# Kernel optimization log

Hardware: AMD Instinct MI355X
Metric: run time of the kernel (lower is better)

The kernel has to match this reference:

```python
import jax, jax.numpy as jnp
import numpy as np

N_NODES = 100000
N_EDGES = 1000000
VOCAB = 128
EMB = 64
HID = 64
N_CLASSES = 2
N_GRAPHS = 2048


def setup_inputs() -> dict:
    key = jax.random.key(0)
    ks = jax.random.split(key, 12)
    x = jax.random.randint(ks[0], (N_NODES,), 0, VOCAB)
    edge_index = jax.random.randint(ks[1], (2, N_EDGES), 0, N_NODES)
    batch = jnp.sort(jax.random.randint(ks[2], (N_NODES,), 0, N_GRAPHS))

    def glorot(k, shape):
        fan = shape[0]
        return jax.random.normal(k, shape, dtype=jnp.float32) / np.sqrt(fan).astype(np.float32)

    emb = jax.random.normal(ks[3], (VOCAB, EMB), dtype=jnp.float32)
    W1_l = glorot(ks[4], (EMB, HID)); b1 = jnp.zeros((HID,), jnp.float32)
    W1_r = glorot(ks[5], (EMB, HID))
    W2_l = glorot(ks[6], (HID, HID)); b2 = jnp.zeros((HID,), jnp.float32)
    W2_r = glorot(ks[7], (HID, HID))
    W_out = glorot(ks[8], (HID, N_CLASSES)); b_out = jnp.zeros((N_CLASSES,), jnp.float32)
    return {"x": x, "edge_index": edge_index, "batch": batch, "emb": emb,
            "W1_l": W1_l, "b1": b1, "W1_r": W1_r,
            "W2_l": W2_l, "b2": b2, "W2_r": W2_r,
            "W_out": W_out, "b_out": b_out}


def _sage_conv(h, src, dst, Wl, bl, Wr):
    # PyG SAGEConv: out = lin_l(mean_{j in N(i)} h_j) + lin_r(h_i); lin_r has no bias
    msgs = h[src]                                                        # [E, D] gather
    agg = jax.ops.segment_sum(msgs, dst, num_segments=N_NODES)          # [N, D] scatter-add
    cnt = jax.ops.segment_sum(jnp.ones((src.shape[0], 1), h.dtype), dst,
                              num_segments=N_NODES)                      # [N, 1] degree
    mean = agg / jnp.maximum(cnt, 1.0)
    return mean @ Wl + bl + h @ Wr


def reference(x, edge_index, batch, emb, W1_l, b1, W1_r, W2_l, b2, W2_r, W_out, b_out):
    src, dst = edge_index[0], edge_index[1]
    h = emb[x]                                                           # [N, EMB]
    h = jax.nn.relu(_sage_conv(h, src, dst, W1_l, b1, W1_r))             # [N, HID]
    h = jax.nn.relu(_sage_conv(h, src, dst, W2_l, b2, W2_r))             # [N, HID]
    # global_mean_pool over graph ids
    gsum = jax.ops.segment_sum(h, batch, num_segments=N_GRAPHS)          # [G, HID]
    gcnt = jax.ops.segment_sum(jnp.ones((N_NODES, 1), h.dtype), batch,
                               num_segments=N_GRAPHS)
    pooled = gsum / jnp.maximum(gcnt, 1.0)
    return pooled @ W_out + b_out                                        # [G, C]
```

## Files before the change

### kernel.cpp

```cpp
#include <hip/hip_runtime.h>
#include <hip/hip_bf16.h>

#define N_NODES 100000
#define N_EDGES 1000000
#define EMB 64
#define HID 64
#define VOCAB 128
#define N_GRAPHS 2048

#define CBUCKET 1024
#define NBK ((N_NODES + CBUCKET - 1) / CBUCKET)
#define CAP 16384
#define CHUNK 4096
#define SCAT_BLOCKS ((N_EDGES + CHUNK - 1) / CHUNK)
#define GB ((N_NODES + 255) / 256)

#define BCASTF(v, l) __int_as_float(__builtin_amdgcn_readlane(__float_as_int(v), (l)))

typedef __attribute__((ext_vector_type(8))) short short8;
typedef __attribute__((ext_vector_type(4))) float f32x4;

__device__ __forceinline__ float bf2f(unsigned short u) {
    return __uint_as_float((unsigned)u << 16);
}
__device__ __forceinline__ unsigned short f2bf(float f) {
    return __bfloat16_as_ushort(__float2bfloat16(f));
}

__global__ __launch_bounds__(256) void setup_kernel(
    const int* __restrict__ batch, int* __restrict__ gstart,
    const float* __restrict__ emb, const float* __restrict__ W1l,
    const float* __restrict__ W1r,
    const float* __restrict__ W2l, const float* __restrict__ W2r,
    float* __restrict__ embW1l, float* __restrict__ embW1r,
    unsigned short* __restrict__ w2frag,
    int* __restrict__ cursor, float* __restrict__ gsum)
{
    int b = blockIdx.x;
    int t = threadIdx.x;
    if (b < GB) {
        int i = b * 256 + t;
        if (i >= N_NODES) return;
        int bg = batch[i];
        int bp = (i == 0) ? -1 : batch[i - 1];
        for (int g = bp + 1; g <= bg; ++g) gstart[g] = i;
        if (i == N_NODES - 1)
            for (int g = bg + 1; g <= N_GRAPHS; ++g) gstart[g] = N_NODES;
    } else if (b < GB + 32) {
        int vb = b - GB;
        int wave = t >> 6, lane = t & 63;
        int v = vb * 4 + wave;
        if (v < VOCAB) {
            float er = emb[v * 64 + lane];
            float al = 0.f, ar = 0.f;
#pragma unroll 8
            for (int d = 0; d < 64; ++d) {
                float e = BCASTF(er, d);
                al += e * W1l[d * 64 + lane];
                ar += e * W1r[d * 64 + lane];
            }
            embW1l[v * 64 + lane] = al;
            embW1r[v * 64 + lane] = ar;
        }
        int g = vb * 256 + t;
        int j = g & 7, l = (g >> 3) & 63, h = (g >> 9) & 1, tt = g >> 10;
        int k = h * 32 + ((l >> 4) * 8) + j;
        int n = tt * 16 + (l & 15);
        float w = (n < 64) ? W2l[k * 64 + n] : W2r[k * 64 + (n - 64)];
        w2frag[g] = f2bf(w);
    } else {
        if (t < NBK) cursor[t] = t * CAP;
        for (int i = t; i < N_GRAPHS * 2; i += 256) gsum[i] = 0.f;
    }
}

__global__ __launch_bounds__(256) void scatter_kernel(
    const int* __restrict__ src, const int* __restrict__ dst,
    int* __restrict__ cursor, unsigned* __restrict__ edge8)
{
    __shared__ unsigned earr[CHUNK];
    __shared__ unsigned char karr[CHUNK];
    __shared__ int bcnt[NBK];
    __shared__ int bbase[NBK];
    int t = threadIdx.x;
    if (t < NBK) bcnt[t] = 0;
    __syncthreads();
    int e0 = blockIdx.x * CHUNK;
    int n = min(e0 + CHUNK, N_EDGES) - e0;
    for (int i = t; i < n; i += 256) {
        int d = dst[e0 + i];
        int s = src[e0 + i];
        int k = d >> 10;
        earr[i] = (unsigned)s | ((unsigned)(d & 1023) << 17);
        karr[i] = (unsigned char)k;
        atomicAdd(&bcnt[k], 1);
    }
    __syncthreads();
    if (t < NBK) {
        int c = bcnt[t];
        bbase[t] = c ? atomicAdd(&cursor[t], c) : 0;
        bcnt[t] = 0;
    }
    __syncthreads();
    for (int i = t; i < n; i += 256) {
        int k = karr[i];
        int off = atomicAdd(&bcnt[k], 1);
        edge8[bbase[k] + off] = earr[i];
    }
}

__global__ __launch_bounds__(256) void csr_kernel(
    const unsigned* __restrict__ edge8, const int* __restrict__ cursor,
    int* __restrict__ row_start, int* __restrict__ deg, int* __restrict__ col)
{
    __shared__ int cnt[CBUCKET];
    __shared__ int ssum[256];
    int b = blockIdx.x;
    int t = threadIdx.x;
    int lo = b * CAP, hi = cursor[b];
    for (int i = t; i < CBUCKET; i += 256) cnt[i] = 0;
    __syncthreads();
    for (int i = lo + t; i < hi; i += 256)
        atomicAdd(&cnt[edge8[i] >> 17], 1);
    __syncthreads();
    int v[4]; int sum = 0;
#pragma unroll
    for (int i = 0; i < 4; ++i) { v[i] = cnt[t * 4 + i]; sum += v[i]; }
    ssum[t] = sum;
    __syncthreads();
    for (int off = 1; off < 256; off <<= 1) {
        int tmp = (t >= off) ? ssum[t - off] : 0;
        __syncthreads();
        ssum[t] += tmp;
        __syncthreads();
    }
    int run = ssum[t] - sum;
    int ex0 = run, ex1 = ex0 + v[0], ex2 = ex1 + v[1], ex3 = ex2 + v[2];
    int node = b * CBUCKET + t * 4;
    if (node + 3 < N_NODES) {
        *(int4*)&row_start[node] = make_int4(lo + ex0, lo + ex1, lo + ex2, lo + ex3);
        *(int4*)&deg[node]       = make_int4(v[0], v[1], v[2], v[3]);
    } else {
        int ex[4] = {ex0, ex1, ex2, ex3};
        for (int i = 0; i < 4; ++i)
            if (node + i < N_NODES) { row_start[node + i] = lo + ex[i]; deg[node + i] = v[i]; }
    }
    cnt[t * 4 + 0] = ex0; cnt[t * 4 + 1] = ex1;
    cnt[t * 4 + 2] = ex2; cnt[t * 4 + 3] = ex3;
    __syncthreads();
    for (int i = lo + t; i < hi; i += 256) {
        unsigned e = edge8[i];
        int slot = atomicAdd(&cnt[e >> 17], 1);
        col[lo + slot] = (int)(e & 0x1FFFF);
    }
}

#define S1_NPW 8
__global__ __launch_bounds__(256) void sage1_kernel(
    const int* __restrict__ x, const float* __restrict__ embW1l,
    const float* __restrict__ embW1r, const float* __restrict__ b1,
    const int* __restrict__ row_start, const int* __restrict__ deg,
    const int* __restrict__ col, unsigned short* __restrict__ h1b)
{
    __shared__ float elds[VOCAB * 64];
    int t = threadIdx.x;
    for (int i = t * 4; i < VOCAB * 64; i += 1024)
        *(float4*)&elds[i] = *(const float4*)&embW1l[i];
    __syncthreads();

    int wave = t >> 6, lane = t & 63;
    int base_node = (blockIdx.x * 4 + wave) * S1_NPW;
    float bias = b1[lane];

    int rs[S1_NPW], dgs[S1_NPW], cidx[S1_NPW], xv[S1_NPW], xn[S1_NPW];
    float self[S1_NPW];
#pragma unroll
    for (int n = 0; n < S1_NPW; ++n) {
        rs[n] = row_start[base_node + n];
        dgs[n] = deg[base_node + n];
        xn[n] = x[base_node + n];
    }
#pragma unroll
    for (int n = 0; n < S1_NPW; ++n)
        cidx[n] = (lane < dgs[n]) ? col[rs[n] + lane] : 0;
#pragma unroll
    for (int n = 0; n < S1_NPW; ++n) {
        xv[n] = (lane < dgs[n]) ? x[cidx[n]] : 0;
        self[n] = embW1r[xn[n] * 64 + lane];
    }

    for (int n = 0; n < S1_NPW; ++n) {
        int node = base_node + n;
        int dg = dgs[n];
        int dgc = (dg < 64) ? dg : 64;

        float s0 = 0.f, s1 = 0.f, s2 = 0.f, s3 = 0.f;
        int j = 0;
        for (; j + 4 <= dgc; j += 4) {
            int x0 = __builtin_amdgcn_readlane(xv[n], j + 0);
            int x1 = __builtin_amdgcn_readlane(xv[n], j + 1);
            int x2 = __builtin_amdgcn_readlane(xv[n], j + 2);
            int x3 = __builtin_amdgcn_readlane(xv[n], j + 3);
            s0 += elds[x0 * 64 + lane];
            s1 += elds[x1 * 64 + lane];
            s2 += elds[x2 * 64 + lane];
            s3 += elds[x3 * 64 + lane];
        }
        for (; j < dgc; ++j) {
            int x0 = __builtin_amdgcn_readlane(xv[n], j);
            s0 += elds[x0 * 64 + lane];
        }
        for (int k = 64; k < dg; ++k) {
            int c = col[rs[n] + k];
            s0 += elds[x[c] * 64 + lane];
        }
        float mean = ((s0 + s1) + (s2 + s3)) / fmaxf((float)dg, 1.0f);
        h1b[node * 64 + lane] = f2bf(fmaxf(mean + bias + self[n], 0.f));
    }
}

__global__ __launch_bounds__(256) void mfma_transform_kernel(
    const unsigned short* __restrict__ h1b,
    const unsigned short* __restrict__ w2frag,
    unsigned char* __restrict__ p8, unsigned short* __restrict__ q16)
{
    int wave = threadIdx.x >> 6, lane = threadIdx.x & 63;
    int base16 = blockIdx.x * 64 + wave * 16;
    if (base16 >= N_NODES) return;
    int m = lane & 15, quad = lane >> 4;

    const unsigned short* arow = h1b + (base16 + m) * 64 + quad * 8;
    short8 a0 = *(const short8*)(arow);
    short8 a1 = *(const short8*)(arow + 32);

#pragma unroll
    for (int tt = 0; tt < 8; ++tt) {
        short8 b0 = *(const short8*)(w2frag + (tt * 1024 + 0)   + lane * 8);
        short8 b1 = *(const short8*)(w2frag + (tt * 1024 + 512) + lane * 8);
        f32x4 acc = {0.f, 0.f, 0.f, 0.f};
        acc = __builtin_amdgcn_mfma_f32_16x16x32_bf16(a0, b0, acc, 0, 0, 0);
        acc = __builtin_amdgcn_mfma_f32_16x16x32_bf16(a1, b1, acc, 0, 0, 0);
        int o = tt * 16 + m;
        if (o < 64) {
            int pk01 = __builtin_amdgcn_cvt_pk_fp8_f32(acc[0], acc[1], 0, false);
            int pk23 = __builtin_amdgcn_cvt_pk_fp8_f32(acc[2], acc[3], 0, false);
            p8[(base16 + quad * 4 + 0) * 64 + o] = (unsigned char)(pk01 & 0xff);
            p8[(base16 + quad * 4 + 1) * 64 + o] = (unsigned char)((pk01 >> 8) & 0xff);
            p8[(base16 + quad * 4 + 2) * 64 + o] = (unsigned char)(pk23 & 0xff);
            p8[(base16 + quad * 4 + 3) * 64 + o] = (unsigned char)((pk23 >> 8) & 0xff);
        } else {
            int oc = o & 63;
#pragma unroll
            for (int i = 0; i < 4; ++i) {
                int node = base16 + quad * 4 + i;
                q16[node * 64 + oc] = f2bf(acc[i]);
            }
        }
    }
}

#define S2_NPW 8
__global__ __launch_bounds__(256, 6) void sage2_kernel(
    const unsigned char* __restrict__ p, const unsigned short* __restrict__ q,
    const int* __restrict__ row_start, const int* __restrict__ deg,
    const int* __restrict__ col, const float* __restrict__ b2,
    const float* __restrict__ Wout, const int* __restrict__ batch,
    float* __restrict__ gsum)
{
    int t = threadIdx.x;
    int wave = t >> 6, lane = t & 63;
    int base_node = (blockIdx.x * 4 + wave) * S2_NPW;
    int c = lane & 15;
    int g = lane >> 4;

    float4 b2v = ((const float4*)b2)[c];
    float4 w01 = ((const float4*)Wout)[c * 2];
    float4 w23 = ((const float4*)Wout)[c * 2 + 1];

    int rs[S2_NPW], dgs[S2_NPW], cidx[S2_NPW];
#pragma unroll
    for (int n = 0; n < S2_NPW; ++n) {
        rs[n] = row_start[base_node + n];
        dgs[n] = deg[base_node + n];
    }
#pragma unroll
    for (int n = 0; n < S2_NPW; ++n)
        cidx[n] = (lane < dgs[n]) ? col[rs[n] + lane] : 0;

    for (int n = 0; n < S2_NPW; ++n) {
        int node = base_node + n;
        int dg = dgs[n];
        int dgc = (dg < 64) ? dg : 64;

        float4 a0 = {0.f,0.f,0.f,0.f}, a1 = {0.f,0.f,0.f,0.f};
        for (int j = 0; j < dgc; j += 8) {
            int jj0 = j + g, jj1 = j + 4 + g;
            int i0 = __shfl(cidx[n], jj0, 64);
            int i1 = __shfl(cidx[n], jj1, 64);
            unsigned v0 = *(const unsigned*)(p + i0 * 64 + c * 4);
            unsigned v1 = *(const unsigned*)(p + i1 * 64 + c * 4);
            if (jj0 < dgc) {
                a0.x += __builtin_amdgcn_cvt_f32_fp8(v0, 0);
                a0.y += __builtin_amdgcn_cvt_f32_fp8(v0, 1);
                a0.z += __builtin_amdgcn_cvt_f32_fp8(v0, 2);
                a0.w += __builtin_amdgcn_cvt_f32_fp8(v0, 3);
            }
            if (jj1 < dgc) {
                a1.x += __builtin_amdgcn_cvt_f32_fp8(v1, 0);
                a1.y += __builtin_amdgcn_cvt_f32_fp8(v1, 1);
                a1.z += __builtin_amdgcn_cvt_f32_fp8(v1, 2);
                a1.w += __builtin_amdgcn_cvt_f32_fp8(v1, 3);
            }
        }
        for (int k = 64; k < dg; ++k) {
            int r = col[rs[n] + k];
            unsigned v = *(const unsigned*)(p + r * 64 + c * 4);
            if (g == 0) {
                a0.x += __builtin_amdgcn_cvt_f32_fp8(v, 0);
                a0.y += __builtin_amdgcn_cvt_f32_fp8(v, 1);
                a0.z += __builtin_amdgcn_cvt_f32_fp8(v, 2);
                a0.w += __builtin_amdgcn_cvt_f32_fp8(v, 3);
            }
        }
        float sx = a0.x + a1.x, sy = a0.y + a1.y, sz = a0.z + a1.z, sw = a0.w + a1.w;
        sx += __shfl_xor(sx, 16, 64); sx += __shfl_xor(sx, 32, 64);
        sy += __shfl_xor(sy, 16, 64); sy += __shfl_xor(sy, 32, 64);
        sz += __shfl_xor(sz, 16, 64); sz += __shfl_xor(sz, 32, 64);
        sw += __shfl_xor(sw, 16, 64); sw += __shfl_xor(sw, 32, 64);

        float inv = 1.0f / fmaxf((float)dg, 1.0f);
        ushort4 qv = *(const ushort4*)(q + node * 64 + c * 4);
        float h0 = fmaxf(sx * inv + b2v.x + bf2f(qv.x), 0.f);
        float h1 = fmaxf(sy * inv + b2v.y + bf2f(qv.y), 0.f);
        float h2 = fmaxf(sz * inv + b2v.z + bf2f(qv.z), 0.f);
        float h3 = fmaxf(sw * inv + b2v.w + bf2f(qv.w), 0.f);

        float p0 = h0 * w01.x + h1 * w01.z + h2 * w23.x + h3 * w23.z;
        float p1 = h0 * w01.y + h1 * w01.w + h2 * w23.y + h3 * w23.w;
        if (g != 0) { p0 = 0.f; p1 = 0.f; }
        p0 += __shfl_down(p0, 8, 64);  p1 += __shfl_down(p1, 8, 64);
        p0 += __shfl_down(p0, 4, 64);  p1 += __shfl_down(p1, 4, 64);
        p0 += __shfl_down(p0, 2, 64);  p1 += __shfl_down(p1, 2, 64);
        p0 += __shfl_down(p0, 1, 64);  p1 += __shfl_down(p1, 1, 64);
        if (lane == 0) {
            int grp = batch[node];
            atomicAdd(&gsum[grp * 2 + 0], p0);
            atomicAdd(&gsum[grp * 2 + 1], p1);
        }
    }
}

__global__ __launch_bounds__(256) void finalize_kernel(
    const float* __restrict__ gsum, const int* __restrict__ gstart,
    const float* __restrict__ bout, float* __restrict__ out)
{
    int g = blockIdx.x * 256 + threadIdx.x;
    if (g >= N_GRAPHS) return;
    int cnt = gstart[g + 1] - gstart[g];
    float inv = 1.0f / fmaxf((float)cnt, 1.0f);
    out[g * 2 + 0] = gsum[g * 2 + 0] * inv + bout[0];
    out[g * 2 + 1] = gsum[g * 2 + 1] * inv + bout[1];
}

extern "C" void kernel_launch(void* const* d_in, const int* in_sizes, int n_in,
                              void* d_out, int out_size, void* d_ws, size_t ws_size,
                              hipStream_t stream) {
    const int*   x    = (const int*)  d_in[0];
    const int*   ei   = (const int*)  d_in[1];
    const int*   batch= (const int*)  d_in[2];
    const float* emb  = (const float*)d_in[3];
    const float* W1l  = (const float*)d_in[4];
    const float* b1   = (const float*)d_in[5];
    const float* W1r  = (const float*)d_in[6];
    const float* W2l  = (const float*)d_in[7];
    const float* b2   = (const float*)d_in[8];
    const float* W2r  = (const float*)d_in[9];
    const float* Wout = (const float*)d_in[10];
    const float* bout = (const float*)d_in[11];
    float* out = (float*)d_out;

    const int* src = ei;
    const int* dst = ei + N_EDGES;

    char* ws = (char*)d_ws;
    size_t off = 0;
    unsigned char*  p8     = (unsigned char*) (ws + off); off += (size_t)N_NODES * 64;
    unsigned short* q16    = (unsigned short*)(ws + off); off += (size_t)N_NODES * 64 * 2;
    unsigned short* h1b    = (unsigned short*)(ws + off); off += (size_t)N_NODES * 64 * 2;
    unsigned short* w2frag = (unsigned short*)(ws + off); off += (size_t)8192 * 2;
    float*    embW1l = (float*)   (ws + off); off += (size_t)VOCAB * 64 * 4;
    float*    embW1r = (float*)   (ws + off); off += (size_t)VOCAB * 64 * 4;
    int*      rowst  = (int*)     (ws + off); off += (size_t)N_NODES * 4;
    int*      deg    = (int*)     (ws + off); off += (size_t)N_NODES * 4;
    int*      col    = (int*)     (ws + off); off += (size_t)(NBK * CAP + 256) * 4;
    unsigned* edge8  = (unsigned*)(ws + off); off += (size_t)NBK * CAP * 4;
    int*      cursor = (int*)     (ws + off); off += (size_t)NBK * 4;
    int*      gstart = (int*)     (ws + off); off += (size_t)(N_GRAPHS + 1) * 4;
    float*    gsum   = (float*)   (ws + off); off += (size_t)N_GRAPHS * 2 * 4;

    setup_kernel<<<GB + 32 + 1, 256, 0, stream>>>(
        batch, gstart, emb, W1l, W1r, W2l, W2r, embW1l, embW1r, w2frag,
        cursor, gsum);
    scatter_kernel<<<SCAT_BLOCKS, 256, 0, stream>>>(src, dst, cursor, edge8);
    csr_kernel<<<NBK, 256, 0, stream>>>(edge8, cursor, rowst, deg, col);
    sage1_kernel<<<N_NODES / (4 * S1_NPW), 256, 0, stream>>>(
        x, embW1l, embW1r, b1, rowst, deg, col, h1b);
    mfma_transform_kernel<<<(N_NODES + 63) / 64, 256, 0, stream>>>(
        h1b, w2frag, p8, q16);
    sage2_kernel<<<N_NODES / (4 * S2_NPW), 256, 0, stream>>>(
        p8, q16, rowst, deg, col, b2, Wout, batch, gsum);
    finalize_kernel<<<(N_GRAPHS + 255) / 256, 256, 0, stream>>>(gsum, gstart, bout, out);
}
```

Baseline: 227.9 us.

## Pack source node vocab id into CSR column entries during scatter

The scatter kernel now looks up x[src] per edge and packs the 7-bit vocab id into the edge record next to the source index and local destination. The record widens to 64 bits. The CSR column array then carries the vocab id in bits 17-23, so sage1 reads it directly instead of doing a dependent gather x[col] per neighbor, and sage2 masks it off. In exchange, scatter does a random gather of x, shared memory for earr doubles, and edge8 traffic between scatter and csr doubles.

```diff
diff --git a/kernel.cpp b/kernel.cpp
--- a/kernel.cpp
+++ b/kernel.cpp
@@ -76,9 +76,10 @@
 
 __global__ __launch_bounds__(256) void scatter_kernel(
     const int* __restrict__ src, const int* __restrict__ dst,
-    int* __restrict__ cursor, unsigned* __restrict__ edge8)
-{
-    __shared__ unsigned earr[CHUNK];
+    const int* __restrict__ x,
+    int* __restrict__ cursor, unsigned long long* __restrict__ edge8)
+{
+    __shared__ unsigned long long earr[CHUNK];
     __shared__ unsigned char karr[CHUNK];
     __shared__ int bcnt[NBK];
     __shared__ int bbase[NBK];
@@ -90,8 +91,11 @@
     for (int i = t; i < n; i += 256) {
         int d = dst[e0 + i];
         int s = src[e0 + i];
+        int xv = x[s];
         int k = d >> 10;
-        earr[i] = (unsigned)s | ((unsigned)(d & 1023) << 17);
+        earr[i] = (unsigned long long)s
+                | ((unsigned long long)xv << 17)
+                | ((unsigned long long)(d & 1023) << 24);
         karr[i] = (unsigned char)k;
         atomicAdd(&bcnt[k], 1);
     }
@@ -110,7 +114,7 @@
 }
 
 __global__ __launch_bounds__(256) void csr_kernel(
-    const unsigned* __restrict__ edge8, const int* __restrict__ cursor,
+    const unsigned long long* __restrict__ edge8, const int* __restrict__ cursor,
     int* __restrict__ row_start, int* __restrict__ deg, int* __restrict__ col)
 {
     __shared__ int cnt[CBUCKET];
@@ -121,7 +125,7 @@
     for (int i = t; i < CBUCKET; i += 256) cnt[i] = 0;
     __syncthreads();
     for (int i = lo + t; i < hi; i += 256)
-        atomicAdd(&cnt[edge8[i] >> 17], 1);
+        atomicAdd(&cnt[(int)(edge8[i] >> 24)], 1);
     __syncthreads();
     int v[4]; int sum = 0;
 #pragma unroll
@@ -149,9 +153,9 @@
     cnt[t * 4 + 2] = ex2; cnt[t * 4 + 3] = ex3;
     __syncthreads();
     for (int i = lo + t; i < hi; i += 256) {
-        unsigned e = edge8[i];
-        int slot = atomicAdd(&cnt[e >> 17], 1);
-        col[lo + slot] = (int)(e & 0x1FFFF);
+        unsigned long long e = edge8[i];
+        int slot = atomicAdd(&cnt[(int)(e >> 24)], 1);
+        col[lo + slot] = (int)(e & 0xFFFFFF);
     }
 }
 
@@ -172,7 +176,7 @@
     int base_node = (blockIdx.x * 4 + wave) * S1_NPW;
     float bias = b1[lane];
 
-    int rs[S1_NPW], dgs[S1_NPW], cidx[S1_NPW], xv[S1_NPW], xn[S1_NPW];
+    int rs[S1_NPW], dgs[S1_NPW], cidx[S1_NPW], xn[S1_NPW];
     float self[S1_NPW];
 #pragma unroll
     for (int n = 0; n < S1_NPW; ++n) {
@@ -181,11 +185,8 @@
         xn[n] = x[base_node + n];
     }
 #pragma unroll
-    for (int n = 0; n < S1_NPW; ++n)
+    for (int n = 0; n < S1_NPW; ++n) {
         cidx[n] = (lane < dgs[n]) ? col[rs[n] + lane] : 0;
-#pragma unroll
-    for (int n = 0; n < S1_NPW; ++n) {
-        xv[n] = (lane < dgs[n]) ? x[cidx[n]] : 0;
         self[n] = embW1r[xn[n] * 64 + lane];
     }
 
@@ -197,22 +198,22 @@
         float s0 = 0.f, s1 = 0.f, s2 = 0.f, s3 = 0.f;
         int j = 0;
         for (; j + 4 <= dgc; j += 4) {
-            int x0 = __builtin_amdgcn_readlane(xv[n], j + 0);
-            int x1 = __builtin_amdgcn_readlane(xv[n], j + 1);
-            int x2 = __builtin_amdgcn_readlane(xv[n], j + 2);
-            int x3 = __builtin_amdgcn_readlane(xv[n], j + 3);
+            int x0 = __builtin_amdgcn_readlane(cidx[n], j + 0) >> 17;
+            int x1 = __builtin_amdgcn_readlane(cidx[n], j + 1) >> 17;
+            int x2 = __builtin_amdgcn_readlane(cidx[n], j + 2) >> 17;
+            int x3 = __builtin_amdgcn_readlane(cidx[n], j + 3) >> 17;
             s0 += elds[x0 * 64 + lane];
             s1 += elds[x1 * 64 + lane];
             s2 += elds[x2 * 64 + lane];
             s3 += elds[x3 * 64 + lane];
         }
         for (; j < dgc; ++j) {
-            int x0 = __builtin_amdgcn_readlane(xv[n], j);
+            int x0 = __builtin_amdgcn_readlane(cidx[n], j) >> 17;
             s0 += elds[x0 * 64 + lane];
         }
         for (int k = 64; k < dg; ++k) {
             int c = col[rs[n] + k];
-            s0 += elds[x[c] * 64 + lane];
+            s0 += elds[(c >> 17) * 64 + lane];
         }
         float mean = ((s0 + s1) + (s2 + s3)) / fmaxf((float)dg, 1.0f);
         h1b[node * 64 + lane] = f2bf(fmaxf(mean + bias + self[n], 0.f));
@@ -285,7 +286,7 @@
     }
 #pragma unroll
     for (int n = 0; n < S2_NPW; ++n)
-        cidx[n] = (lane < dgs[n]) ? col[rs[n] + lane] : 0;
+        cidx[n] = (lane < dgs[n]) ? (col[rs[n] + lane] & 0x1FFFF) : 0;
 
     for (int n = 0; n < S2_NPW; ++n) {
         int node = base_node + n;
@@ -313,7 +314,7 @@
             }
         }
         for (int k = 64; k < dg; ++k) {
-            int r = col[rs[n] + k];
+            int r = col[rs[n] + k] & 0x1FFFF;
             unsigned v = *(const unsigned*)(p + r * 64 + c * 4);
             if (g == 0) {
                 a0.x += __builtin_amdgcn_cvt_f32_fp8(v, 0);
@@ -393,7 +394,9 @@
     int*      rowst  = (int*)     (ws + off); off += (size_t)N_NODES * 4;
     int*      deg    = (int*)     (ws + off); off += (size_t)N_NODES * 4;
     int*      col    = (int*)     (ws + off); off += (size_t)(NBK * CAP + 256) * 4;
-    unsigned* edge8  = (unsigned*)(ws + off); off += (size_t)NBK * CAP * 4;
+    off = (off + 7) & ~(size_t)7;
+    unsigned long long* edge8 = (unsigned long long*)(ws + off);
+    off += (size_t)NBK * CAP * 8;
     int*      cursor = (int*)     (ws + off); off += (size_t)NBK * 4;
     int*      gstart = (int*)     (ws + off); off += (size_t)(N_GRAPHS + 1) * 4;
     float*    gsum   = (float*)   (ws + off); off += (size_t)N_GRAPHS * 2 * 4;
@@ -401,7 +404,7 @@
     setup_kernel<<<GB + 32 + 1, 256, 0, stream>>>(
         batch, gstart, emb, W1l, W1r, W2l, W2r, embW1l, embW1r, w2frag,
         cursor, gsum);
-    scatter_kernel<<<SCAT_BLOCKS, 256, 0, stream>>>(src, dst, cursor, edge8);
+    scatter_kernel<<<SCAT_BLOCKS, 256, 0, stream>>>(src, dst, x, cursor, edge8);
     csr_kernel<<<NBK, 256, 0, stream>>>(edge8, cursor, rowst, deg, col);
     sage1_kernel<<<N_NODES / (4 * S1_NPW), 256, 0, stream>>>(
         x, embW1l, embW1r, b1, rowst, deg, col, h1b);
```

Result: no change. 228.7 us (+0.4%).
